# Optimization experiments

Hardware: AMD Instinct MI355X
Metric: run time of the kernel (lower is better)

The kernel has to match this reference:

```python
import jax, jax.numpy as jnp
import numpy as np

N_NODES = 50000
N_EDGES = 800000
NODE_DIM = 128
EDGE_DIM = 16
HIDDEN = 64


def _gcn_conv(x, W, b, src, dst, n_nodes):
    """PyG-style GCNConv: add self-loops, symmetric deg^-1/2 normalization,
    aggregate messages from src into dst, then add bias. x: [N, Fin]."""
    h = x @ W  # [N, Fout]
    loops = jnp.arange(n_nodes)
    s = jnp.concatenate([src, loops])  # sources incl. self-loops
    d = jnp.concatenate([dst, loops])  # targets incl. self-loops
    deg = jax.ops.segment_sum(jnp.ones_like(d, dtype=h.dtype), d, num_segments=n_nodes)
    dinv = jax.lax.rsqrt(jnp.maximum(deg, 1.0))  # deg >= 1 thanks to self-loops
    norm = dinv[s] * dinv[d]  # [E+N]
    msg = h[s] * norm[:, None]  # gather + scale
    out = jax.ops.segment_sum(msg, d, num_segments=n_nodes)  # scatter-add
    return out + b


def setup_inputs() -> dict:
    key = jax.random.key(0)
    ks = jax.random.split(key, 12)
    x = jax.random.normal(ks[0], (N_NODES, NODE_DIM), dtype=jnp.float32)
    edge_index = jax.random.randint(ks[1], (2, N_EDGES), 0, N_NODES, dtype=jnp.int64)
    edge_attr = jax.random.normal(ks[2], (N_EDGES, EDGE_DIM), dtype=jnp.float32)
    def glorot(k, fan_in, fan_out):
        s = float(np.sqrt(2.0 / (fan_in + fan_out)))
        return jax.random.normal(k, (fan_in, fan_out), dtype=jnp.float32) * s
    W1 = glorot(ks[3], NODE_DIM, HIDDEN)
    b1 = jnp.zeros((HIDDEN,), jnp.float32)
    W2 = glorot(ks[4], HIDDEN, HIDDEN)
    b2 = jnp.zeros((HIDDEN,), jnp.float32)
    Wm1 = glorot(ks[5], 2 * HIDDEN + EDGE_DIM, HIDDEN)
    bm1 = jnp.zeros((HIDDEN,), jnp.float32)
    Wm2 = glorot(ks[6], HIDDEN, 2)
    bm2 = jnp.zeros((2,), jnp.float32)
    return {"x": x, "edge_index": edge_index, "edge_attr": edge_attr,
            "W1": W1, "b1": b1, "W2": W2, "b2": b2,
            "Wm1": Wm1, "bm1": bm1, "Wm2": Wm2, "bm2": bm2}


def reference(x, edge_index, edge_attr, W1, b1, W2, b2, Wm1, bm1, Wm2, bm2):
    n = x.shape[0]
    src, dst = edge_index[0], edge_index[1]
    h = jax.nn.relu(_gcn_conv(x, W1, b1, src, dst, n))
    h = jax.nn.relu(_gcn_conv(h, W2, b2, src, dst, n))
    # gather endpoint embeddings + concat edge features -> edge MLP
    edge_embed = jnp.concatenate([h[src], h[dst], edge_attr], axis=1)  # [E, 2H+Fe]
    out = jax.nn.relu(edge_embed @ Wm1 + bm1) @ Wm2 + bm2  # [E, 2]
    return out
```

## Files before the change

### kernel.cpp

```cpp
#include <hip/hip_runtime.h>
#include <hip/hip_fp16.h>


typedef float v4f __attribute__((ext_vector_type(4)));
typedef _Float16 v4h __attribute__((ext_vector_type(4)));

__device__ __forceinline__ void fma4(float4& a, float s, const float4& b) {
    a.x = fmaf(s, b.x, a.x);
    a.y = fmaf(s, b.y, a.y);
    a.z = fmaf(s, b.z, a.z);
    a.w = fmaf(s, b.w, a.w);
}

__device__ __forceinline__ float4 relu4(float4 v) {
    v.x = fmaxf(v.x, 0.f); v.y = fmaxf(v.y, 0.f);
    v.z = fmaxf(v.z, 0.f); v.w = fmaxf(v.w, 0.f);
    return v;
}

__device__ __forceinline__ void store4(float* C, size_t idx, float4 v) {
    *reinterpret_cast<float4*>(C + idx) = v;
}
__device__ __forceinline__ void store4(__half* C, size_t idx, float4 v) {
    __half2 lo = __floats2half2_rn(v.x, v.y);
    __half2 hi = __floats2half2_rn(v.z, v.w);
    uint2 raw;
    raw.x = *reinterpret_cast<unsigned*>(&lo);
    raw.y = *reinterpret_cast<unsigned*>(&hi);
    *reinterpret_cast<uint2*>(C + idx) = raw;
}

__device__ __forceinline__ void load_lds16(const void* g, void* l) {
    __builtin_amdgcn_global_load_lds(
        (const __attribute__((address_space(1))) void*)g,
        (__attribute__((address_space(3))) void*)l, 16, 0, 0);
}

__global__ void k_count(const int* __restrict__ dst, int* __restrict__ cnt,
                        int* __restrict__ rank, int E) {
    int e = blockIdx.x * 256 + threadIdx.x;
    if (e < E) rank[e] = atomicAdd(&cnt[dst[e]], 1);
}

__global__ void k_bsum(const int* __restrict__ cnt, int* __restrict__ bsum,
                       float* __restrict__ dinv, int N) {
    int i = blockIdx.x * 256 + threadIdx.x;
    int v = (i < N) ? cnt[i] : 0;
    if (i < N) dinv[i] = rsqrtf((float)v + 1.0f);
    int r = v;
#pragma unroll
    for (int d = 1; d < 64; d <<= 1) r += __shfl_xor(r, d);
    __shared__ int ws[4];
    if ((threadIdx.x & 63) == 0) ws[threadIdx.x >> 6] = r;
    __syncthreads();
    if (threadIdx.x == 0) bsum[blockIdx.x] = ws[0] + ws[1] + ws[2] + ws[3];
}

__global__ void k_scanb(int* __restrict__ bsum, int nb) {
    int t = threadIdx.x;
    int lane = t & 63, w = t >> 6;
    int v = (t < nb) ? bsum[t] : 0;
    int x = v;
#pragma unroll
    for (int d = 1; d < 64; d <<= 1) {
        int y = __shfl_up(x, d);
        if (lane >= d) x += y;
    }
    __shared__ int ws[4];
    if (lane == 63) ws[w] = x;
    __syncthreads();
    int woff = 0;
    for (int j = 0; j < w; j++) woff += ws[j];
    if (t < nb) bsum[t] = woff + x - v;
}

__global__ void k_scan3(const int* __restrict__ cnt, const int* __restrict__ bsum,
                        int* __restrict__ row_ptr, int N, int E) {
    int t = threadIdx.x, b = blockIdx.x;
    int i = b * 256 + t;
    int lane = t & 63, w = t >> 6;
    int v = (i < N) ? cnt[i] : 0;
    int x = v;
#pragma unroll
    for (int d = 1; d < 64; d <<= 1) {
        int y = __shfl_up(x, d);
        if (lane >= d) x += y;
    }
    __shared__ int ws[4];
    if (lane == 63) ws[w] = x;
    __syncthreads();
    int woff = 0;
    for (int j = 0; j < w; j++) woff += ws[j];
    if (i < N) row_ptr[i] = bsum[b] + woff + x - v;
    if (i == 0) row_ptr[N] = E;
}

__global__ void k_fill(const int* __restrict__ src, const int* __restrict__ dst,
                       const int* __restrict__ row_ptr, const int* __restrict__ rank,
                       int* __restrict__ csr_src, int E) {
    int e = blockIdx.x * 256 + threadIdx.x;
    if (e >= E) return;
    csr_src[row_ptr[dst[e]] + rank[e]] = src[e];
}

template<int K, bool RELU_A, bool SCALE, typename OutT>
__global__ __launch_bounds__(256) void k_gemm(const float* __restrict__ A,
                                              const float* __restrict__ B,
                                              const float* __restrict__ dinv,
                                              OutT* __restrict__ C, int M) {
    constexpr int AS = K + 4;
    __shared__ float As[32 * AS];
    __shared__ float Bs[64 * 64];
    const int t = threadIdx.x;
    const int r0 = blockIdx.x * 32;

    constexpr int C4 = K / 4;
    for (int idx = t; idx < 32 * C4; idx += 256) {
        int row = idx / C4, c4 = idx % C4;
        float4 v = make_float4(0.f, 0.f, 0.f, 0.f);
        if (r0 + row < M)
            v = reinterpret_cast<const float4*>(A + (size_t)(r0 + row) * K)[c4];
        if (RELU_A) v = relu4(v);
        *reinterpret_cast<float4*>(&As[row * AS + 4 * c4]) = v;
    }

    const int tx = t & 15, ty = t >> 4;
    float4 acc[2];
    acc[0] = acc[1] = make_float4(0.f, 0.f, 0.f, 0.f);

    for (int c = 0; c < K / 64; c++) {
        __syncthreads();
        for (int idx = t; idx < 64 * 16; idx += 256)
            reinterpret_cast<float4*>(Bs)[idx] =
                reinterpret_cast<const float4*>(B + (size_t)c * 64 * 64)[idx];
        __syncthreads();
#pragma unroll 4
        for (int k0 = 0; k0 < 64; k0 += 4) {
            float4 b0 = *reinterpret_cast<const float4*>(&Bs[(k0 + 0) * 64 + 4 * tx]);
            float4 b1 = *reinterpret_cast<const float4*>(&Bs[(k0 + 1) * 64 + 4 * tx]);
            float4 b2 = *reinterpret_cast<const float4*>(&Bs[(k0 + 2) * 64 + 4 * tx]);
            float4 b3 = *reinterpret_cast<const float4*>(&Bs[(k0 + 3) * 64 + 4 * tx]);
#pragma unroll
            for (int i = 0; i < 2; i++) {
                float4 a = *reinterpret_cast<const float4*>(
                    &As[(2 * ty + i) * AS + c * 64 + k0]);
                fma4(acc[i], a.x, b0);
                fma4(acc[i], a.y, b1);
                fma4(acc[i], a.z, b2);
                fma4(acc[i], a.w, b3);
            }
        }
    }

#pragma unroll
    for (int i = 0; i < 2; i++) {
        int row = r0 + 2 * ty + i;
        if (row < M) {
            float4 o = acc[i];
            if (SCALE) {
                float di = dinv[row];
                o = make_float4(di * o.x, di * o.y, di * o.z, di * o.w);
            }
            store4(C, (size_t)row * 64 + 4 * tx, o);
        }
    }
}

__global__ __launch_bounds__(256) void k_proj(const float* __restrict__ A,
                                              const float* __restrict__ B0,
                                              const float* __restrict__ B1,
                                              const float* __restrict__ bias,
                                              __half* __restrict__ C0,
                                              __half* __restrict__ C1, int M) {
    constexpr int AS = 68;
    __shared__ float As[32 * AS];
    __shared__ float Bs[64 * 64];
    const int t = threadIdx.x;
    const int r0 = blockIdx.x * 32;

    for (int idx = t; idx < 32 * 16; idx += 256) {
        int row = idx / 16, c4 = idx % 16;
        float4 v = make_float4(0.f, 0.f, 0.f, 0.f);
        if (r0 + row < M)
            v = relu4(reinterpret_cast<const float4*>(A + (size_t)(r0 + row) * 64)[c4]);
        *reinterpret_cast<float4*>(&As[row * AS + 4 * c4]) = v;
    }

    const int tx = t & 15, ty = t >> 4;
    const float4 bb = *reinterpret_cast<const float4*>(&bias[4 * tx]);
    for (int m = 0; m < 2; m++) {
        const float* B = m ? B1 : B0;
        __half* C = m ? C1 : C0;
        __syncthreads();
        for (int idx = t; idx < 64 * 16; idx += 256)
            reinterpret_cast<float4*>(Bs)[idx] =
                reinterpret_cast<const float4*>(B)[idx];
        __syncthreads();
        float4 acc[2];
        acc[0] = acc[1] = make_float4(0.f, 0.f, 0.f, 0.f);
#pragma unroll 4
        for (int k0 = 0; k0 < 64; k0 += 4) {
            float4 b0 = *reinterpret_cast<const float4*>(&Bs[(k0 + 0) * 64 + 4 * tx]);
            float4 b1 = *reinterpret_cast<const float4*>(&Bs[(k0 + 1) * 64 + 4 * tx]);
            float4 b2 = *reinterpret_cast<const float4*>(&Bs[(k0 + 2) * 64 + 4 * tx]);
            float4 b3 = *reinterpret_cast<const float4*>(&Bs[(k0 + 3) * 64 + 4 * tx]);
#pragma unroll
            for (int i = 0; i < 2; i++) {
                float4 a = *reinterpret_cast<const float4*>(&As[(2 * ty + i) * AS + k0]);
                fma4(acc[i], a.x, b0);
                fma4(acc[i], a.y, b1);
                fma4(acc[i], a.z, b2);
                fma4(acc[i], a.w, b3);
            }
        }
#pragma unroll
        for (int i = 0; i < 2; i++) {
            int row = r0 + 2 * ty + i;
            if (row < M) {
                float4 o = acc[i];
                if (m == 0) {
                    o.x += bb.x; o.y += bb.y; o.z += bb.z; o.w += bb.w;
                }
                store4(C, (size_t)row * 64 + 4 * tx, o);
            }
        }
    }
}

__global__ __launch_bounds__(256, 4) void k_agg(const __half* __restrict__ A16,
                                                const int* __restrict__ row_ptr,
                                                const int* __restrict__ csr_src,
                                                const float* __restrict__ dinv,
                                                const float* __restrict__ bias,
                                                float* __restrict__ out, int N) {
    int gw = (blockIdx.x * 256 + threadIdx.x) >> 6;
    int sub = (threadIdx.x >> 4) & 3;
    int l = threadIdx.x & 15;
    int node = gw * 4 + sub;
    if (node >= N) return;
    const uint2* A4 = reinterpret_cast<const uint2*>(A16);

    int beg = row_ptr[node], end = row_ptr[node + 1];
    uint2 selfv = A4[(size_t)node * 16 + l];
    float2 a0 = __half22float2(*reinterpret_cast<__half2*>(&selfv.x));
    float2 a1 = __half22float2(*reinterpret_cast<__half2*>(&selfv.y));
    float4 acc = make_float4(a0.x, a0.y, a1.x, a1.y);

#define ACC(u)                                                          \
    {                                                                   \
        float2 f0 = __half22float2(*reinterpret_cast<__half2*>(&u.x));  \
        float2 f1 = __half22float2(*reinterpret_cast<__half2*>(&u.y));  \
        acc.x += f0.x; acc.y += f0.y; acc.z += f1.x; acc.w += f1.y;     \
    }
    for (int p = beg; p < end; p += 16) {
        int m = min(16, end - p);
        int sl = (p + l < end) ? csr_src[p + l] : 0;
        int j = 0;
        for (; j + 7 < m; j += 8) {
            uint2 u0 = A4[(size_t)__shfl(sl, j + 0, 16) * 16 + l];
            uint2 u1 = A4[(size_t)__shfl(sl, j + 1, 16) * 16 + l];
            uint2 u2 = A4[(size_t)__shfl(sl, j + 2, 16) * 16 + l];
            uint2 u3 = A4[(size_t)__shfl(sl, j + 3, 16) * 16 + l];
            uint2 u4 = A4[(size_t)__shfl(sl, j + 4, 16) * 16 + l];
            uint2 u5 = A4[(size_t)__shfl(sl, j + 5, 16) * 16 + l];
            uint2 u6 = A4[(size_t)__shfl(sl, j + 6, 16) * 16 + l];
            uint2 u7 = A4[(size_t)__shfl(sl, j + 7, 16) * 16 + l];
            ACC(u0) ACC(u1) ACC(u2) ACC(u3) ACC(u4) ACC(u5) ACC(u6) ACC(u7)
        }
        for (; j + 3 < m; j += 4) {
            uint2 u0 = A4[(size_t)__shfl(sl, j + 0, 16) * 16 + l];
            uint2 u1 = A4[(size_t)__shfl(sl, j + 1, 16) * 16 + l];
            uint2 u2 = A4[(size_t)__shfl(sl, j + 2, 16) * 16 + l];
            uint2 u3 = A4[(size_t)__shfl(sl, j + 3, 16) * 16 + l];
            ACC(u0) ACC(u1) ACC(u2) ACC(u3)
        }
        for (; j < m; j++) {
            uint2 u0 = A4[(size_t)__shfl(sl, j, 16) * 16 + l];
            ACC(u0)
        }
    }
#undef ACC
    float di = dinv[node];
    float4 bb = *reinterpret_cast<const float4*>(&bias[4 * l]);
    float4 o = make_float4(fmaf(di, acc.x, bb.x), fmaf(di, acc.y, bb.y),
                           fmaf(di, acc.z, bb.z), fmaf(di, acc.w, bb.w));
    *reinterpret_cast<float4*>(&out[(size_t)node * 64 + 4 * l]) = o;
}

__global__ __launch_bounds__(256, 4) void k_edge(
    const __half* __restrict__ Ps, const __half* __restrict__ Pd,
    const int* __restrict__ src, const int* __restrict__ dst,
    const float* __restrict__ ea, const float* __restrict__ We,
    const float* __restrict__ Wm2, const float* __restrict__ bm2,
    float* __restrict__ out, int E) {
    __shared__ __align__(16) char smem[4 * 12288];
    const int lane = threadIdx.x & 63;
    const int wid = (blockIdx.x * 256 + threadIdx.x) >> 6;
    const int li = lane & 15, g = lane >> 4;
    const int e0 = wid * 64;
    if (e0 >= E) return;

    char* wbase = smem + (threadIdx.x >> 6) * 12288;
    const float4* ea4 = reinterpret_cast<const float4*>(ea);

    v4h af[4];
#pragma unroll
    for (int m = 0; m < 4; m++) {
        v4h a;
#pragma unroll
        for (int i = 0; i < 4; i++)
            a[i] = (_Float16)We[(4 * g + i) * 64 + 16 * m + li];
        af[m] = a;
    }

    float4 w2lo[4], w2hi[4];
#pragma unroll
    for (int m = 0; m < 4; m++) {
        int dim0 = 16 * m + 4 * g;
        w2lo[m] = *reinterpret_cast<const float4*>(&Wm2[2 * dim0]);
        w2hi[m] = *reinterpret_cast<const float4*>(&Wm2[2 * dim0 + 4]);
    }
    const float c0 = bm2[0], c1 = bm2[1];

    const int ecl = min(e0 + lane, E - 1);
    const int sv = src[ecl], dv = dst[ecl];

    v4h bh[4];
#pragma unroll
    for (int n = 0; n < 4; n++) {
        int ee = min(e0 + 16 * n + li, E - 1);
        float4 bf = ea4[(size_t)ee * 4 + g];
        v4h t;
        t[0] = (_Float16)bf.x; t[1] = (_Float16)bf.y;
        t[2] = (_Float16)bf.z; t[3] = (_Float16)bf.w;
        bh[n] = t;
    }

    const int jrow = lane >> 3;
    const int csw = (lane & 7) ^ jrow;

#define STAGE(n, b)                                                              \
    {                                                                            \
        char* lb = wbase + (b) * 4096 + lane * 16;                               \
        int n0 = __shfl(sv, 16 * (n) + jrow);                                    \
        int n1 = __shfl(sv, 16 * (n) + 8 + jrow);                                \
        int n2 = __shfl(dv, 16 * (n) + jrow);                                    \
        int n3 = __shfl(dv, 16 * (n) + 8 + jrow);                                \
        load_lds16((const char*)Ps + (size_t)n0 * 128 + (csw << 4), lb);         \
        load_lds16((const char*)Ps + (size_t)n1 * 128 + (csw << 4), lb + 1024);  \
        load_lds16((const char*)Pd + (size_t)n2 * 128 + (csw << 4), lb + 2048);  \
        load_lds16((const char*)Pd + (size_t)n3 * 128 + (csw << 4), lb + 3072);  \
    }

    float p0s[4], p1s[4];

#define COMPUTE(n, b)                                                             \
    {                                                                             \
        const char* rb = wbase + (b) * 4096;                                      \
        uint2 us[4], ud[4];                                                       \
        _Pragma("unroll")                                                         \
        for (int m = 0; m < 4; m++) {                                             \
            int q = 4 * m + g;                                                    \
            int off = li * 128 + ((((q >> 1) ^ (li & 7)) << 4) | ((q & 1) << 3)); \
            us[m] = *reinterpret_cast<const uint2*>(rb + off);                    \
            ud[m] = *reinterpret_cast<const uint2*>(rb + 2048 + off);             \
        }                                                                         \
        float p0 = 0.f, p1 = 0.f;                                                 \
        _Pragma("unroll")                                                         \
        for (int m = 0; m < 4; m++) {                                             \
            float2 s0 = __half22float2(*reinterpret_cast<__half2*>(&us[m].x));    \
            float2 s1 = __half22float2(*reinterpret_cast<__half2*>(&us[m].y));    \
            float2 d0 = __half22float2(*reinterpret_cast<__half2*>(&ud[m].x));    \
            float2 d1 = __half22float2(*reinterpret_cast<__half2*>(&ud[m].y));    \
            v4f c;                                                                \
            c[0] = s0.x + d0.x;                                                   \
            c[1] = s0.y + d0.y;                                                   \
            c[2] = s1.x + d1.x;                                                   \
            c[3] = s1.y + d1.y;                                                   \
            v4f q = __builtin_amdgcn_mfma_f32_16x16x16f16(af[m], bh[n], c, 0, 0, 0); \
            float u0 = fmaxf(q[0], 0.f), u1 = fmaxf(q[1], 0.f);                   \
            float u2 = fmaxf(q[2], 0.f), u3 = fmaxf(q[3], 0.f);                   \
            p0 += u0 * w2lo[m].x + u1 * w2lo[m].z + u2 * w2hi[m].x + u3 * w2hi[m].z; \
            p1 += u0 * w2lo[m].y + u1 * w2lo[m].w + u2 * w2hi[m].y + u3 * w2hi[m].w; \
        }                                                                         \
        p0 += __shfl_xor(p0, 16); p0 += __shfl_xor(p0, 32);                       \
        p1 += __shfl_xor(p1, 16); p1 += __shfl_xor(p1, 32);                       \
        p0s[n] = p0; p1s[n] = p1;                                                 \
    }

    STAGE(0, 0)
    STAGE(1, 1)
    STAGE(2, 2)
    asm volatile("s_waitcnt vmcnt(8)" ::: "memory");
    COMPUTE(0, 0)
    STAGE(3, 0)
    asm volatile("s_waitcnt vmcnt(8)" ::: "memory");
    COMPUTE(1, 1)
    asm volatile("s_waitcnt vmcnt(4)" ::: "memory");
    COMPUTE(2, 2)
    asm volatile("s_waitcnt vmcnt(0)" ::: "memory");
    COMPUTE(3, 0)
#undef STAGE
#undef COMPUTE

    if (g == 0) {
#pragma unroll
        for (int n = 0; n < 4; n++) {
            int e = e0 + 16 * n + li;
            if (e < E)
                *reinterpret_cast<float2*>(&out[(size_t)e * 2]) =
                    make_float2(p0s[n] + c0, p1s[n] + c1);
        }
    }
}

static inline size_t align256(size_t x) { return (x + 255) & ~(size_t)255; }

extern "C" void kernel_launch(void* const* d_in, const int* in_sizes, int n_in,
                              void* d_out, int out_size, void* d_ws, size_t ws_size,
                              hipStream_t stream) {
    const float* x = (const float*)d_in[0];
    const int* ei = (const int*)d_in[1];
    const float* ea = (const float*)d_in[2];
    const float* W1 = (const float*)d_in[3];
    const float* b1 = (const float*)d_in[4];
    const float* W2 = (const float*)d_in[5];
    const float* b2 = (const float*)d_in[6];
    const float* Wm1 = (const float*)d_in[7];
    const float* bm1 = (const float*)d_in[8];
    const float* Wm2 = (const float*)d_in[9];
    const float* bm2 = (const float*)d_in[10];

    const int N = in_sizes[0] / 128;
    const int E = in_sizes[1] / 2;
    const int* src = ei;
    const int* dst = ei + E;
    float* out = (float*)d_out;

    const int NB = (N + 255) / 256;

    char* p = (char*)d_ws;
    int* cnt = (int*)p;        p += align256((size_t)N * 4);
    int* rank = (int*)p;       p += align256((size_t)E * 4);
    int* row_ptr = (int*)p;    p += align256((size_t)(N + 1) * 4);
    int* bsum = (int*)p;       p += align256((size_t)NB * 4);
    int* csr_src = (int*)p;    p += align256((size_t)E * 4);
    float* dinv = (float*)p;   p += align256((size_t)N * 4);
    __half* A16 = (__half*)p;  p += align256((size_t)N * 64 * 2);
    float* B = (float*)p;      p += align256((size_t)N * 64 * 4);
    __half* Ps16 = (__half*)p; p += align256((size_t)N * 64 * 2);
    __half* Pd16 = (__half*)p;

    hipMemsetAsync(cnt, 0, (size_t)N * sizeof(int), stream);
    k_count<<<(E + 255) / 256, 256, 0, stream>>>(dst, cnt, rank, E);
    k_bsum<<<NB, 256, 0, stream>>>(cnt, bsum, dinv, N);
    k_scanb<<<1, 256, 0, stream>>>(bsum, NB);
    k_scan3<<<NB, 256, 0, stream>>>(cnt, bsum, row_ptr, N, E);
    k_fill<<<(E + 255) / 256, 256, 0, stream>>>(src, dst, row_ptr, rank, csr_src, E);

    k_gemm<128, false, true, __half><<<(N + 31) / 32, 256, 0, stream>>>(
        x, W1, dinv, A16, N);
    k_agg<<<(N + 15) / 16, 256, 0, stream>>>(A16, row_ptr, csr_src, dinv, b1, B, N);

    k_gemm<64, true, true, __half><<<(N + 31) / 32, 256, 0, stream>>>(
        B, W2, dinv, A16, N);
    k_agg<<<(N + 15) / 16, 256, 0, stream>>>(A16, row_ptr, csr_src, dinv, b2, B, N);

    k_proj<<<(N + 31) / 32, 256, 0, stream>>>(B, Wm1, Wm1 + 64 * 64, bm1,
                                              Ps16, Pd16, N);
    int waves = (E + 63) / 64;
    k_edge<<<(waves + 3) / 4, 256, 0, stream>>>(Ps16, Pd16, src, dst, ea,
                                                Wm1 + 128 * 64, Wm2, bm2,
                                                out, E);
}
```

Measured before the change: 289.7 us.

## Process edges in dst-sorted CSR order in edge MLP kernel

k_fill now also records (dst, original edge id) per CSR slot, and the edge kernel walks edges in destination-sorted order instead of original order. Consecutive edges then share destination nodes, so Pd row gathers should hit cache more often. In exchange, edge_attr reads and output writes become scattered by original edge id, and k_fill writes an extra 8 bytes per edge.

```diff
diff --git a/kernel.cpp b/kernel.cpp
--- a/kernel.cpp
+++ b/kernel.cpp
@@ -97,10 +97,13 @@
 
 __global__ void k_fill(const int* __restrict__ src, const int* __restrict__ dst,
                        const int* __restrict__ row_ptr, const int* __restrict__ rank,
-                       int* __restrict__ csr_src, int E) {
+                       int* __restrict__ csr_src, int2* __restrict__ csr_de, int E) {
     int e = blockIdx.x * 256 + threadIdx.x;
     if (e >= E) return;
-    csr_src[row_ptr[dst[e]] + rank[e]] = src[e];
+    int d = dst[e];
+    int pos = row_ptr[d] + rank[e];
+    csr_src[pos] = src[e];
+    csr_de[pos] = make_int2(d, e);
 }
 
 template<int K, bool RELU_A, bool SCALE, typename OutT>
@@ -289,7 +292,7 @@
 
 __global__ __launch_bounds__(256, 4) void k_edge(
     const __half* __restrict__ Ps, const __half* __restrict__ Pd,
-    const int* __restrict__ src, const int* __restrict__ dst,
+    const int* __restrict__ csr_src, const int2* __restrict__ csr_de,
     const float* __restrict__ ea, const float* __restrict__ We,
     const float* __restrict__ Wm2, const float* __restrict__ bm2,
     float* __restrict__ out, int E) {
@@ -297,8 +300,8 @@
     const int lane = threadIdx.x & 63;
     const int wid = (blockIdx.x * 256 + threadIdx.x) >> 6;
     const int li = lane & 15, g = lane >> 4;
-    const int e0 = wid * 64;
-    if (e0 >= E) return;
+    const int p0 = wid * 64;
+    if (p0 >= E) return;
 
     char* wbase = smem + (threadIdx.x >> 6) * 12288;
     const float4* ea4 = reinterpret_cast<const float4*>(ea);
@@ -322,14 +325,18 @@
     }
     const float c0 = bm2[0], c1 = bm2[1];
 
-    const int ecl = min(e0 + lane, E - 1);
-    const int sv = src[ecl], dv = dst[ecl];
+    const int pcl = min(p0 + lane, E - 1);
+    const int sv = csr_src[pcl];
+    const int2 de = csr_de[pcl];
+    const int dv = de.x, ev = de.y;
 
     v4h bh[4];
+    int eo[4];
 #pragma unroll
     for (int n = 0; n < 4; n++) {
-        int ee = min(e0 + 16 * n + li, E - 1);
-        float4 bf = ea4[(size_t)ee * 4 + g];
+        int eid = __shfl(ev, 16 * n + li);
+        eo[n] = eid;
+        float4 bf = ea4[(size_t)eid * 4 + g];
         v4h t;
         t[0] = (_Float16)bf.x; t[1] = (_Float16)bf.y;
         t[2] = (_Float16)bf.z; t[3] = (_Float16)bf.w;
@@ -365,7 +372,7 @@
             us[m] = *reinterpret_cast<const uint2*>(rb + off);                    \
             ud[m] = *reinterpret_cast<const uint2*>(rb + 2048 + off);             \
         }                                                                         \
-        float p0 = 0.f, p1 = 0.f;                                                 \
+        float p0_ = 0.f, p1_ = 0.f;                                               \
         _Pragma("unroll")                                                         \
         for (int m = 0; m < 4; m++) {                                             \
             float2 s0 = __half22float2(*reinterpret_cast<__half2*>(&us[m].x));    \
@@ -380,12 +387,12 @@
             v4f q = __builtin_amdgcn_mfma_f32_16x16x16f16(af[m], bh[n], c, 0, 0, 0); \
             float u0 = fmaxf(q[0], 0.f), u1 = fmaxf(q[1], 0.f);                   \
             float u2 = fmaxf(q[2], 0.f), u3 = fmaxf(q[3], 0.f);                   \
-            p0 += u0 * w2lo[m].x + u1 * w2lo[m].z + u2 * w2hi[m].x + u3 * w2hi[m].z; \
-            p1 += u0 * w2lo[m].y + u1 * w2lo[m].w + u2 * w2hi[m].y + u3 * w2hi[m].w; \
+            p0_ += u0 * w2lo[m].x + u1 * w2lo[m].z + u2 * w2hi[m].x + u3 * w2hi[m].z; \
+            p1_ += u0 * w2lo[m].y + u1 * w2lo[m].w + u2 * w2hi[m].y + u3 * w2hi[m].w; \
         }                                                                         \
-        p0 += __shfl_xor(p0, 16); p0 += __shfl_xor(p0, 32);                       \
-        p1 += __shfl_xor(p1, 16); p1 += __shfl_xor(p1, 32);                       \
-        p0s[n] = p0; p1s[n] = p1;                                                 \
+        p0_ += __shfl_xor(p0_, 16); p0_ += __shfl_xor(p0_, 32);                   \
+        p1_ += __shfl_xor(p1_, 16); p1_ += __shfl_xor(p1_, 32);                   \
+        p0s[n] = p0_; p1s[n] = p1_;                                               \
     }
 
     STAGE(0, 0)
@@ -406,9 +413,9 @@
     if (g == 0) {
 #pragma unroll
         for (int n = 0; n < 4; n++) {
-            int e = e0 + 16 * n + li;
-            if (e < E)
-                *reinterpret_cast<float2*>(&out[(size_t)e * 2]) =
+            int pos = p0 + 16 * n + li;
+            if (pos < E)
+                *reinterpret_cast<float2*>(&out[(size_t)eo[n] * 2]) =
                     make_float2(p0s[n] + c0, p1s[n] + c1);
         }
     }
@@ -445,6 +452,7 @@
     int* row_ptr = (int*)p;    p += align256((size_t)(N + 1) * 4);
     int* bsum = (int*)p;       p += align256((size_t)NB * 4);
     int* csr_src = (int*)p;    p += align256((size_t)E * 4);
+    int2* csr_de = (int2*)p;   p += align256((size_t)E * 8);
     float* dinv = (float*)p;   p += align256((size_t)N * 4);
     __half* A16 = (__half*)p;  p += align256((size_t)N * 64 * 2);
     float* B = (float*)p;      p += align256((size_t)N * 64 * 4);
@@ -456,7 +464,8 @@
     k_bsum<<<NB, 256, 0, stream>>>(cnt, bsum, dinv, N);
     k_scanb<<<1, 256, 0, stream>>>(bsum, NB);
     k_scan3<<<NB, 256, 0, stream>>>(cnt, bsum, row_ptr, N, E);
-    k_fill<<<(E + 255) / 256, 256, 0, stream>>>(src, dst, row_ptr, rank, csr_src, E);
+    k_fill<<<(E + 255) / 256, 256, 0, stream>>>(src, dst, row_ptr, rank,
+                                                csr_src, csr_de, E);
 
     k_gemm<128, false, true, __half><<<(N + 31) / 32, 256, 0, stream>>>(
         x, W1, dinv, A16, N);
@@ -469,7 +478,7 @@
     k_proj<<<(N + 31) / 32, 256, 0, stream>>>(B, Wm1, Wm1 + 64 * 64, bm1,
                                               Ps16, Pd16, N);
     int waves = (E + 63) / 64;
-    k_edge<<<(waves + 3) / 4, 256, 0, stream>>>(Ps16, Pd16, src, dst, ea,
+    k_edge<<<(waves + 3) / 4, 256, 0, stream>>>(Ps16, Pd16, csr_src, csr_de, ea,
                                                 Wm1 + 128 * 64, Wm2, bm2,
                                                 out, E);
 }
```

New measurement: 320.9 us. 1.11x slower.

## Split GCN features into two 32-column halves and aggregate each separately

Applied to the files above, without the earlier changes.

The GEMM now writes its fp16 output as two separate [N,32] arrays. Each aggregation then runs as two passes, one per half, with 8 lanes per node instead of 16. The goal is to shrink the working set of each gather pass (3.2 MB instead of 6.4 MB) so more of it stays in cache during random neighbor gathers. The cost is reading the CSR indices twice and launching extra kernels, with shorter 64-byte row segments per gather.

```diff
diff --git a/kernel.cpp b/kernel.cpp
--- a/kernel.cpp
+++ b/kernel.cpp
@@ -103,11 +103,12 @@
     csr_src[row_ptr[dst[e]] + rank[e]] = src[e];
 }
 
-template<int K, bool RELU_A, bool SCALE, typename OutT>
+template<int K, bool RELU_A, bool SCALE, bool SPLIT, typename OutT>
 __global__ __launch_bounds__(256) void k_gemm(const float* __restrict__ A,
                                               const float* __restrict__ B,
                                               const float* __restrict__ dinv,
-                                              OutT* __restrict__ C, int M) {
+                                              OutT* __restrict__ C,
+                                              OutT* __restrict__ C2, int M) {
     constexpr int AS = K + 4;
     __shared__ float As[32 * AS];
     __shared__ float Bs[64 * 64];
@@ -161,7 +162,12 @@
                 float di = dinv[row];
                 o = make_float4(di * o.x, di * o.y, di * o.z, di * o.w);
             }
-            store4(C, (size_t)row * 64 + 4 * tx, o);
+            if (SPLIT) {
+                OutT* P = (tx < 8) ? C : C2;
+                store4(P, (size_t)row * 32 + 4 * (tx & 7), o);
+            } else {
+                store4(C, (size_t)row * 64 + 4 * tx, o);
+            }
         }
     }
 }
@@ -227,21 +233,22 @@
     }
 }
 
-__global__ __launch_bounds__(256, 4) void k_agg(const __half* __restrict__ A16,
-                                                const int* __restrict__ row_ptr,
-                                                const int* __restrict__ csr_src,
-                                                const float* __restrict__ dinv,
-                                                const float* __restrict__ bias,
-                                                float* __restrict__ out, int N) {
+__global__ __launch_bounds__(256, 4) void k_agg32(const __half* __restrict__ A,
+                                                  const int* __restrict__ row_ptr,
+                                                  const int* __restrict__ csr_src,
+                                                  const float* __restrict__ dinv,
+                                                  const float* __restrict__ bias,
+                                                  int boff,
+                                                  float* __restrict__ out, int N) {
     int gw = (blockIdx.x * 256 + threadIdx.x) >> 6;
-    int sub = (threadIdx.x >> 4) & 3;
-    int l = threadIdx.x & 15;
-    int node = gw * 4 + sub;
+    int sub = (threadIdx.x >> 3) & 7;
+    int l = threadIdx.x & 7;
+    int node = gw * 8 + sub;
     if (node >= N) return;
-    const uint2* A4 = reinterpret_cast<const uint2*>(A16);
+    const uint2* A2 = reinterpret_cast<const uint2*>(A);
 
     int beg = row_ptr[node], end = row_ptr[node + 1];
-    uint2 selfv = A4[(size_t)node * 16 + l];
+    uint2 selfv = A2[(size_t)node * 8 + l];
     float2 a0 = __half22float2(*reinterpret_cast<__half2*>(&selfv.x));
     float2 a1 = __half22float2(*reinterpret_cast<__half2*>(&selfv.y));
     float4 acc = make_float4(a0.x, a0.y, a1.x, a1.y);
@@ -252,39 +259,39 @@
         float2 f1 = __half22float2(*reinterpret_cast<__half2*>(&u.y));  \
         acc.x += f0.x; acc.y += f0.y; acc.z += f1.x; acc.w += f1.y;     \
     }
-    for (int p = beg; p < end; p += 16) {
-        int m = min(16, end - p);
+    for (int p = beg; p < end; p += 8) {
+        int m = min(8, end - p);
         int sl = (p + l < end) ? csr_src[p + l] : 0;
         int j = 0;
         for (; j + 7 < m; j += 8) {
-            uint2 u0 = A4[(size_t)__shfl(sl, j + 0, 16) * 16 + l];
-            uint2 u1 = A4[(size_t)__shfl(sl, j + 1, 16) * 16 + l];
-            uint2 u2 = A4[(size_t)__shfl(sl, j + 2, 16) * 16 + l];
-            uint2 u3 = A4[(size_t)__shfl(sl, j + 3, 16) * 16 + l];
-            uint2 u4 = A4[(size_t)__shfl(sl, j + 4, 16) * 16 + l];
-            uint2 u5 = A4[(size_t)__shfl(sl, j + 5, 16) * 16 + l];
-            uint2 u6 = A4[(size_t)__shfl(sl, j + 6, 16) * 16 + l];
-            uint2 u7 = A4[(size_t)__shfl(sl, j + 7, 16) * 16 + l];
+            uint2 u0 = A2[(size_t)__shfl(sl, j + 0, 8) * 8 + l];
+            uint2 u1 = A2[(size_t)__shfl(sl, j + 1, 8) * 8 + l];
+            uint2 u2 = A2[(size_t)__shfl(sl, j + 2, 8) * 8 + l];
+            uint2 u3 = A2[(size_t)__shfl(sl, j + 3, 8) * 8 + l];
+            uint2 u4 = A2[(size_t)__shfl(sl, j + 4, 8) * 8 + l];
+            uint2 u5 = A2[(size_t)__shfl(sl, j + 5, 8) * 8 + l];
+            uint2 u6 = A2[(size_t)__shfl(sl, j + 6, 8) * 8 + l];
+            uint2 u7 = A2[(size_t)__shfl(sl, j + 7, 8) * 8 + l];
             ACC(u0) ACC(u1) ACC(u2) ACC(u3) ACC(u4) ACC(u5) ACC(u6) ACC(u7)
         }
         for (; j + 3 < m; j += 4) {
-            uint2 u0 = A4[(size_t)__shfl(sl, j + 0, 16) * 16 + l];
-            uint2 u1 = A4[(size_t)__shfl(sl, j + 1, 16) * 16 + l];
-            uint2 u2 = A4[(size_t)__shfl(sl, j + 2, 16) * 16 + l];
-            uint2 u3 = A4[(size_t)__shfl(sl, j + 3, 16) * 16 + l];
+            uint2 u0 = A2[(size_t)__shfl(sl, j + 0, 8) * 8 + l];
+            uint2 u1 = A2[(size_t)__shfl(sl, j + 1, 8) * 8 + l];
+            uint2 u2 = A2[(size_t)__shfl(sl, j + 2, 8) * 8 + l];
+            uint2 u3 = A2[(size_t)__shfl(sl, j + 3, 8) * 8 + l];
             ACC(u0) ACC(u1) ACC(u2) ACC(u3)
         }
         for (; j < m; j++) {
-            uint2 u0 = A4[(size_t)__shfl(sl, j, 16) * 16 + l];
+            uint2 u0 = A2[(size_t)__shfl(sl, j, 8) * 8 + l];
             ACC(u0)
         }
     }
 #undef ACC
     float di = dinv[node];
-    float4 bb = *reinterpret_cast<const float4*>(&bias[4 * l]);
+    float4 bb = *reinterpret_cast<const float4*>(&bias[boff + 4 * l]);
     float4 o = make_float4(fmaf(di, acc.x, bb.x), fmaf(di, acc.y, bb.y),
                            fmaf(di, acc.z, bb.z), fmaf(di, acc.w, bb.w));
-    *reinterpret_cast<float4*>(&out[(size_t)node * 64 + 4 * l]) = o;
+    *reinterpret_cast<float4*>(&out[(size_t)node * 64 + boff + 4 * l]) = o;
 }
 
 __global__ __launch_bounds__(256, 4) void k_edge(
@@ -365,7 +372,7 @@
             us[m] = *reinterpret_cast<const uint2*>(rb + off);                    \
             ud[m] = *reinterpret_cast<const uint2*>(rb + 2048 + off);             \
         }                                                                         \
-        float p0 = 0.f, p1 = 0.f;                                                 \
+        float p0_ = 0.f, p1_ = 0.f;                                               \
         _Pragma("unroll")                                                         \
         for (int m = 0; m < 4; m++) {                                             \
             float2 s0 = __half22float2(*reinterpret_cast<__half2*>(&us[m].x));    \
@@ -380,12 +387,12 @@
             v4f q = __builtin_amdgcn_mfma_f32_16x16x16f16(af[m], bh[n], c, 0, 0, 0); \
             float u0 = fmaxf(q[0], 0.f), u1 = fmaxf(q[1], 0.f);                   \
             float u2 = fmaxf(q[2], 0.f), u3 = fmaxf(q[3], 0.f);                   \
-            p0 += u0 * w2lo[m].x + u1 * w2lo[m].z + u2 * w2hi[m].x + u3 * w2hi[m].z; \
-            p1 += u0 * w2lo[m].y + u1 * w2lo[m].w + u2 * w2hi[m].y + u3 * w2hi[m].w; \
+            p0_ += u0 * w2lo[m].x + u1 * w2lo[m].z + u2 * w2hi[m].x + u3 * w2hi[m].z; \
+            p1_ += u0 * w2lo[m].y + u1 * w2lo[m].w + u2 * w2hi[m].y + u3 * w2hi[m].w; \
         }                                                                         \
-        p0 += __shfl_xor(p0, 16); p0 += __shfl_xor(p0, 32);                       \
-        p1 += __shfl_xor(p1, 16); p1 += __shfl_xor(p1, 32);                       \
-        p0s[n] = p0; p1s[n] = p1;                                                 \
+        p0_ += __shfl_xor(p0_, 16); p0_ += __shfl_xor(p0_, 32);                   \
+        p1_ += __shfl_xor(p1_, 16); p1_ += __shfl_xor(p1_, 32);                   \
+        p0s[n] = p0_; p1s[n] = p1_;                                               \
     }
 
     STAGE(0, 0)
@@ -440,15 +447,16 @@
     const int NB = (N + 255) / 256;
 
     char* p = (char*)d_ws;
-    int* cnt = (int*)p;        p += align256((size_t)N * 4);
-    int* rank = (int*)p;       p += align256((size_t)E * 4);
-    int* row_ptr = (int*)p;    p += align256((size_t)(N + 1) * 4);
-    int* bsum = (int*)p;       p += align256((size_t)NB * 4);
-    int* csr_src = (int*)p;    p += align256((size_t)E * 4);
-    float* dinv = (float*)p;   p += align256((size_t)N * 4);
-    __half* A16 = (__half*)p;  p += align256((size_t)N * 64 * 2);
-    float* B = (float*)p;      p += align256((size_t)N * 64 * 4);
-    __half* Ps16 = (__half*)p; p += align256((size_t)N * 64 * 2);
+    int* cnt = (int*)p;         p += align256((size_t)N * 4);
+    int* rank = (int*)p;        p += align256((size_t)E * 4);
+    int* row_ptr = (int*)p;     p += align256((size_t)(N + 1) * 4);
+    int* bsum = (int*)p;        p += align256((size_t)NB * 4);
+    int* csr_src = (int*)p;     p += align256((size_t)E * 4);
+    float* dinv = (float*)p;    p += align256((size_t)N * 4);
+    __half* A16a = (__half*)p;  p += align256((size_t)N * 32 * 2);
+    __half* A16b = (__half*)p;  p += align256((size_t)N * 32 * 2);
+    float* B = (float*)p;       p += align256((size_t)N * 64 * 4);
+    __half* Ps16 = (__half*)p;  p += align256((size_t)N * 64 * 2);
     __half* Pd16 = (__half*)p;
 
     hipMemsetAsync(cnt, 0, (size_t)N * sizeof(int), stream);
@@ -458,13 +466,17 @@
     k_scan3<<<NB, 256, 0, stream>>>(cnt, bsum, row_ptr, N, E);
     k_fill<<<(E + 255) / 256, 256, 0, stream>>>(src, dst, row_ptr, rank, csr_src, E);
 
-    k_gemm<128, false, true, __half><<<(N + 31) / 32, 256, 0, stream>>>(
-        x, W1, dinv, A16, N);
-    k_agg<<<(N + 15) / 16, 256, 0, stream>>>(A16, row_ptr, csr_src, dinv, b1, B, N);
-
-    k_gemm<64, true, true, __half><<<(N + 31) / 32, 256, 0, stream>>>(
-        B, W2, dinv, A16, N);
-    k_agg<<<(N + 15) / 16, 256, 0, stream>>>(A16, row_ptr, csr_src, dinv, b2, B, N);
+    const int AGG_B = (N + 31) / 32;
+
+    k_gemm<128, false, true, true, __half><<<(N + 31) / 32, 256, 0, stream>>>(
+        x, W1, dinv, A16a, A16b, N);
+    k_agg32<<<AGG_B, 256, 0, stream>>>(A16a, row_ptr, csr_src, dinv, b1, 0, B, N);
+    k_agg32<<<AGG_B, 256, 0, stream>>>(A16b, row_ptr, csr_src, dinv, b1, 32, B, N);
+
+    k_gemm<64, true, true, true, __half><<<(N + 31) / 32, 256, 0, stream>>>(
+        B, W2, dinv, A16a, A16b, N);
+    k_agg32<<<AGG_B, 256, 0, stream>>>(A16a, row_ptr, csr_src, dinv, b2, 0, B, N);
+    k_agg32<<<AGG_B, 256, 0, stream>>>(A16b, row_ptr, csr_src, dinv, b2, 32, B, N);
 
     k_proj<<<(N + 31) / 32, 256, 0, stream>>>(B, Wm1, Wm1 + 64 * 64, bm1,
                                               Ps16, Pd16, N);
```

Result: slower. 312.0 us (+7.7%).

## Replace fp32 SIMT GEMMs with a unified fp16 MFMA GEMM kernel

Applied to the files above, without the earlier changes.

Replaces the scalar-FMA k_gemm and k_proj kernels with one templated k_mgemm. It converts A and a transposed B to fp16 in LDS and computes with mfma_f32_16x16x16f16 on 64-row tiles. The same kernel can produce two outputs, so the dual projection, bias add and dinv scaling are all handled in one place. It aims to cut ALU and LDS cost in the three dense GEMMs. In exchange the inputs are rounded to fp16, the transposed LDS writes may cause bank conflicts, and the epilogue does narrow 2-byte strided stores.

```diff
diff --git a/kernel.cpp b/kernel.cpp
--- a/kernel.cpp
+++ b/kernel.cpp
@@ -4,30 +4,11 @@
 
 typedef float v4f __attribute__((ext_vector_type(4)));
 typedef _Float16 v4h __attribute__((ext_vector_type(4)));
-
-__device__ __forceinline__ void fma4(float4& a, float s, const float4& b) {
-    a.x = fmaf(s, b.x, a.x);
-    a.y = fmaf(s, b.y, a.y);
-    a.z = fmaf(s, b.z, a.z);
-    a.w = fmaf(s, b.w, a.w);
-}
 
 __device__ __forceinline__ float4 relu4(float4 v) {
     v.x = fmaxf(v.x, 0.f); v.y = fmaxf(v.y, 0.f);
     v.z = fmaxf(v.z, 0.f); v.w = fmaxf(v.w, 0.f);
     return v;
-}
-
-__device__ __forceinline__ void store4(float* C, size_t idx, float4 v) {
-    *reinterpret_cast<float4*>(C + idx) = v;
-}
-__device__ __forceinline__ void store4(__half* C, size_t idx, float4 v) {
-    __half2 lo = __floats2half2_rn(v.x, v.y);
-    __half2 hi = __floats2half2_rn(v.z, v.w);
-    uint2 raw;
-    raw.x = *reinterpret_cast<unsigned*>(&lo);
-    raw.y = *reinterpret_cast<unsigned*>(&hi);
-    *reinterpret_cast<uint2*>(C + idx) = raw;
 }
 
 __device__ __forceinline__ void load_lds16(const void* g, void* l) {
@@ -103,125 +84,85 @@
     csr_src[row_ptr[dst[e]] + rank[e]] = src[e];
 }
 
-template<int K, bool RELU_A, bool SCALE, typename OutT>
-__global__ __launch_bounds__(256) void k_gemm(const float* __restrict__ A,
-                                              const float* __restrict__ B,
-                                              const float* __restrict__ dinv,
-                                              OutT* __restrict__ C, int M) {
-    constexpr int AS = K + 4;
-    __shared__ float As[32 * AS];
-    __shared__ float Bs[64 * 64];
+template<int K, bool RELU_A, bool SCALE, int NB>
+__global__ __launch_bounds__(256) void k_mgemm(
+    const float* __restrict__ A, const float* __restrict__ B0,
+    const float* __restrict__ B1, const float* __restrict__ bias,
+    const float* __restrict__ dinv, __half* __restrict__ C0,
+    __half* __restrict__ C1, int M) {
+    constexpr int P = K + 8;
+    __shared__ __half As[64 * P];
+    __shared__ __half Bs[NB * 64 * P];
     const int t = threadIdx.x;
-    const int r0 = blockIdx.x * 32;
+    const int r0 = blockIdx.x * 64;
 
     constexpr int C4 = K / 4;
-    for (int idx = t; idx < 32 * C4; idx += 256) {
+    for (int idx = t; idx < 64 * C4; idx += 256) {
         int row = idx / C4, c4 = idx % C4;
         float4 v = make_float4(0.f, 0.f, 0.f, 0.f);
         if (r0 + row < M)
             v = reinterpret_cast<const float4*>(A + (size_t)(r0 + row) * K)[c4];
         if (RELU_A) v = relu4(v);
-        *reinterpret_cast<float4*>(&As[row * AS + 4 * c4]) = v;
-    }
-
-    const int tx = t & 15, ty = t >> 4;
-    float4 acc[2];
-    acc[0] = acc[1] = make_float4(0.f, 0.f, 0.f, 0.f);
-
-    for (int c = 0; c < K / 64; c++) {
-        __syncthreads();
-        for (int idx = t; idx < 64 * 16; idx += 256)
-            reinterpret_cast<float4*>(Bs)[idx] =
-                reinterpret_cast<const float4*>(B + (size_t)c * 64 * 64)[idx];
-        __syncthreads();
-#pragma unroll 4
-        for (int k0 = 0; k0 < 64; k0 += 4) {
-            float4 b0 = *reinterpret_cast<const float4*>(&Bs[(k0 + 0) * 64 + 4 * tx]);
-            float4 b1 = *reinterpret_cast<const float4*>(&Bs[(k0 + 1) * 64 + 4 * tx]);
-            float4 b2 = *reinterpret_cast<const float4*>(&Bs[(k0 + 2) * 64 + 4 * tx]);
-            float4 b3 = *reinterpret_cast<const float4*>(&Bs[(k0 + 3) * 64 + 4 * tx]);
-#pragma unroll
-            for (int i = 0; i < 2; i++) {
-                float4 a = *reinterpret_cast<const float4*>(
-                    &As[(2 * ty + i) * AS + c * 64 + k0]);
-                fma4(acc[i], a.x, b0);
-                fma4(acc[i], a.y, b1);
-                fma4(acc[i], a.z, b2);
-                fma4(acc[i], a.w, b3);
+        __half* d = &As[row * P + 4 * c4];
+        d[0] = __float2half(v.x); d[1] = __float2half(v.y);
+        d[2] = __float2half(v.z); d[3] = __float2half(v.w);
+    }
+    for (int m = 0; m < NB; m++) {
+        const float* Bm = m ? B1 : B0;
+        __half* Bsm = &Bs[m * 64 * P];
+        for (int idx = t; idx < K * 16; idx += 256) {
+            int k = idx >> 4, c4 = idx & 15;
+            float4 v = reinterpret_cast<const float4*>(Bm + (size_t)k * 64)[c4];
+            Bsm[(4 * c4 + 0) * P + k] = __float2half(v.x);
+            Bsm[(4 * c4 + 1) * P + k] = __float2half(v.y);
+            Bsm[(4 * c4 + 2) * P + k] = __float2half(v.z);
+            Bsm[(4 * c4 + 3) * P + k] = __float2half(v.w);
+        }
+    }
+    __syncthreads();
+
+    const int lane = t & 63, w = t >> 6;
+    const int li = lane & 15, g = lane >> 4;
+
+    v4f acc[NB][4];
+    const v4f zero = {0.f, 0.f, 0.f, 0.f};
+#pragma unroll
+    for (int m = 0; m < NB; m++)
+#pragma unroll
+        for (int c = 0; c < 4; c++) acc[m][c] = zero;
+
+#pragma unroll
+    for (int kk = 0; kk < K; kk += 16) {
+        v4h a = *reinterpret_cast<const v4h*>(&As[(16 * w + li) * P + kk + 4 * g]);
+#pragma unroll
+        for (int m = 0; m < NB; m++) {
+#pragma unroll
+            for (int c = 0; c < 4; c++) {
+                v4h b = *reinterpret_cast<const v4h*>(
+                    &Bs[m * 64 * P + (16 * c + li) * P + kk + 4 * g]);
+                acc[m][c] =
+                    __builtin_amdgcn_mfma_f32_16x16x16f16(a, b, acc[m][c], 0, 0, 0);
             }
         }
     }
 
-#pragma unroll
-    for (int i = 0; i < 2; i++) {
-        int row = r0 + 2 * ty + i;
-        if (row < M) {
-            float4 o = acc[i];
-            if (SCALE) {
-                float di = dinv[row];
-                o = make_float4(di * o.x, di * o.y, di * o.z, di * o.w);
-            }
-            store4(C, (size_t)row * 64 + 4 * tx, o);
-        }
-    }
-}
-
-__global__ __launch_bounds__(256) void k_proj(const float* __restrict__ A,
-                                              const float* __restrict__ B0,
-                                              const float* __restrict__ B1,
-                                              const float* __restrict__ bias,
-                                              __half* __restrict__ C0,
-                                              __half* __restrict__ C1, int M) {
-    constexpr int AS = 68;
-    __shared__ float As[32 * AS];
-    __shared__ float Bs[64 * 64];
-    const int t = threadIdx.x;
-    const int r0 = blockIdx.x * 32;
-
-    for (int idx = t; idx < 32 * 16; idx += 256) {
-        int row = idx / 16, c4 = idx % 16;
-        float4 v = make_float4(0.f, 0.f, 0.f, 0.f);
-        if (r0 + row < M)
-            v = relu4(reinterpret_cast<const float4*>(A + (size_t)(r0 + row) * 64)[c4]);
-        *reinterpret_cast<float4*>(&As[row * AS + 4 * c4]) = v;
-    }
-
-    const int tx = t & 15, ty = t >> 4;
-    const float4 bb = *reinterpret_cast<const float4*>(&bias[4 * tx]);
-    for (int m = 0; m < 2; m++) {
-        const float* B = m ? B1 : B0;
+    const int rbase = r0 + 16 * w + 4 * g;
+    float4 dv = make_float4(1.f, 1.f, 1.f, 1.f);
+    if (SCALE) dv = *reinterpret_cast<const float4*>(&dinv[rbase]);
+    const float sc[4] = {dv.x, dv.y, dv.z, dv.w};
+#pragma unroll
+    for (int m = 0; m < NB; m++) {
         __half* C = m ? C1 : C0;
-        __syncthreads();
-        for (int idx = t; idx < 64 * 16; idx += 256)
-            reinterpret_cast<float4*>(Bs)[idx] =
-                reinterpret_cast<const float4*>(B)[idx];
-        __syncthreads();
-        float4 acc[2];
-        acc[0] = acc[1] = make_float4(0.f, 0.f, 0.f, 0.f);
-#pragma unroll 4
-        for (int k0 = 0; k0 < 64; k0 += 4) {
-            float4 b0 = *reinterpret_cast<const float4*>(&Bs[(k0 + 0) * 64 + 4 * tx]);
-            float4 b1 = *reinterpret_cast<const float4*>(&Bs[(k0 + 1) * 64 + 4 * tx]);
-            float4 b2 = *reinterpret_cast<const float4*>(&Bs[(k0 + 2) * 64 + 4 * tx]);
-            float4 b3 = *reinterpret_cast<const float4*>(&Bs[(k0 + 3) * 64 + 4 * tx]);
-#pragma unroll
-            for (int i = 0; i < 2; i++) {
-                float4 a = *reinterpret_cast<const float4*>(&As[(2 * ty + i) * AS + k0]);
-                fma4(acc[i], a.x, b0);
-                fma4(acc[i], a.y, b1);
-                fma4(acc[i], a.z, b2);
-                fma4(acc[i], a.w, b3);
-            }
-        }
-#pragma unroll
-        for (int i = 0; i < 2; i++) {
-            int row = r0 + 2 * ty + i;
-            if (row < M) {
-                float4 o = acc[i];
-                if (m == 0) {
-                    o.x += bb.x; o.y += bb.y; o.z += bb.z; o.w += bb.w;
-                }
-                store4(C, (size_t)row * 64 + 4 * tx, o);
+#pragma unroll
+        for (int c = 0; c < 4; c++) {
+            int col = 16 * c + li;
+            float badd = (NB == 2 && m == 0) ? bias[col] : 0.f;
+#pragma unroll
+            for (int r = 0; r < 4; r++) {
+                int gr = rbase + r;
+                if (gr < M)
+                    C[(size_t)gr * 64 + col] =
+                        __float2half(acc[m][c][r] * sc[r] + badd);
             }
         }
     }
@@ -365,7 +306,7 @@
             us[m] = *reinterpret_cast<const uint2*>(rb + off);                    \
             ud[m] = *reinterpret_cast<const uint2*>(rb + 2048 + off);             \
         }                                                                         \
-        float p0 = 0.f, p1 = 0.f;                                                 \
+        float p0_ = 0.f, p1_ = 0.f;                                               \
         _Pragma("unroll")                                                         \
         for (int m = 0; m < 4; m++) {                                             \
             float2 s0 = __half22float2(*reinterpret_cast<__half2*>(&us[m].x));    \
@@ -380,12 +321,12 @@
             v4f q = __builtin_amdgcn_mfma_f32_16x16x16f16(af[m], bh[n], c, 0, 0, 0); \
             float u0 = fmaxf(q[0], 0.f), u1 = fmaxf(q[1], 0.f);                   \
             float u2 = fmaxf(q[2], 0.f), u3 = fmaxf(q[3], 0.f);                   \
-            p0 += u0 * w2lo[m].x + u1 * w2lo[m].z + u2 * w2hi[m].x + u3 * w2hi[m].z; \
-            p1 += u0 * w2lo[m].y + u1 * w2lo[m].w + u2 * w2hi[m].y + u3 * w2hi[m].w; \
+            p0_ += u0 * w2lo[m].x + u1 * w2lo[m].z + u2 * w2hi[m].x + u3 * w2hi[m].z; \
+            p1_ += u0 * w2lo[m].y + u1 * w2lo[m].w + u2 * w2hi[m].y + u3 * w2hi[m].w; \
         }                                                                         \
-        p0 += __shfl_xor(p0, 16); p0 += __shfl_xor(p0, 32);                       \
-        p1 += __shfl_xor(p1, 16); p1 += __shfl_xor(p1, 32);                       \
-        p0s[n] = p0; p1s[n] = p1;                                                 \
+        p0_ += __shfl_xor(p0_, 16); p0_ += __shfl_xor(p0_, 32);                   \
+        p1_ += __shfl_xor(p1_, 16); p1_ += __shfl_xor(p1_, 32);                   \
+        p0s[n] = p0_; p1s[n] = p1_;                                               \
     }
 
     STAGE(0, 0)
@@ -458,16 +399,18 @@
     k_scan3<<<NB, 256, 0, stream>>>(cnt, bsum, row_ptr, N, E);
     k_fill<<<(E + 255) / 256, 256, 0, stream>>>(src, dst, row_ptr, rank, csr_src, E);
 
-    k_gemm<128, false, true, __half><<<(N + 31) / 32, 256, 0, stream>>>(
-        x, W1, dinv, A16, N);
+    const int GB = (N + 63) / 64;
+
+    k_mgemm<128, false, true, 1><<<GB, 256, 0, stream>>>(
+        x, W1, nullptr, nullptr, dinv, A16, nullptr, N);
     k_agg<<<(N + 15) / 16, 256, 0, stream>>>(A16, row_ptr, csr_src, dinv, b1, B, N);
 
-    k_gemm<64, true, true, __half><<<(N + 31) / 32, 256, 0, stream>>>(
-        B, W2, dinv, A16, N);
+    k_mgemm<64, true, true, 1><<<GB, 256, 0, stream>>>(
+        B, W2, nullptr, nullptr, dinv, A16, nullptr, N);
     k_agg<<<(N + 15) / 16, 256, 0, stream>>>(A16, row_ptr, csr_src, dinv, b2, B, N);
 
-    k_proj<<<(N + 31) / 32, 256, 0, stream>>>(B, Wm1, Wm1 + 64 * 64, bm1,
-                                              Ps16, Pd16, N);
+    k_mgemm<64, true, false, 2><<<GB, 256, 0, stream>>>(
+        B, Wm1, Wm1 + 64 * 64, bm1, nullptr, Ps16, Pd16, N);
     int waves = (E + 63) / 64;
     k_edge<<<(waves + 3) / 4, 256, 0, stream>>>(Ps16, Pd16, src, dst, ea,
                                                 Wm1 + 128 * 64, Wm2, bm2,
```

Result: faster. 276.4 us (-4.6%).
